# Kernel tuning notes

Hardware: AMD Instinct MI355X
Metric: run time of the kernel (lower is better)

The kernel has to match this reference:

```python
import jax, jax.numpy as jnp
import numpy as np

TEMPERATURE = 0.1
SINGLE_POS = False
EPS = 1e-8  # torch CosineSimilarity eps
B, D = 8192, 128
N_DATA = 100000


def setup_inputs() -> dict:
    key = jax.random.key(0)
    k1, k2, k3, k4 = jax.random.split(key, 4)
    features = jax.random.normal(k1, (B, D), dtype=jnp.float32)
    data_ix = jax.random.randint(k2, (B,), 0, N_DATA, dtype=jnp.int64)
    targets_t = jax.random.randint(k3, (N_DATA,), 0, 2, dtype=jnp.int64)
    targets_p = jax.random.randint(k4, (N_DATA,), 0, 2, dtype=jnp.int64)
    return {"features": features, "data_ix": data_ix,
            "targets_t": targets_t, "targets_p": targets_p}


def reference(features, data_ix, targets_t, targets_p):
    tt = targets_t[data_ix]  # [B]
    tp = targets_p[data_ix]  # [B]

    # cosine similarity matrix [B, B] (torch CosineSimilarity semantics)
    norms = jnp.linalg.norm(features, axis=1)  # [B]
    dots = features @ features.T               # [B, B]
    sim = dots / jnp.maximum(norms[:, None] * norms[None, :], EPS)
    logits = sim / TEMPERATURE                 # log(exp(sim/T)) == sim/T
    exp_sim = jnp.exp(logits)

    # pos: same true label, different predicted label; neg: reversed
    same_t = tt[:, None] == tt[None, :]
    same_p = tp[:, None] == tp[None, :]
    pos_mask = same_t & ~same_p   # excludes self automatically
    neg_mask = ~same_t & same_p

    pos_cnt = pos_mask.sum(axis=1)  # [B]
    neg_cnt = neg_mask.sum(axis=1)  # [B]

    exp_pos_sum = jnp.sum(jnp.where(pos_mask, exp_sim, 0.0), axis=1)  # [B]
    exp_neg_sum = jnp.sum(jnp.where(neg_mask, exp_sim, 0.0), axis=1)  # [B]

    if SINGLE_POS:
        # per-pair denominator: log(exp_neg_sum + exp_pos_ij)
        log_denom = jnp.log(exp_neg_sum[:, None] + exp_sim)  # [B, B]
        log_probs_sum = jnp.sum(jnp.where(pos_mask, logits - log_denom, 0.0), axis=1)
    else:
        log_denom = jnp.log(exp_neg_sum + exp_pos_sum)  # [B]
        log_probs_sum = jnp.sum(jnp.where(pos_mask, logits - log_denom[:, None], 0.0), axis=1)

    valid = (pos_cnt > 0) & (neg_cnt > 0)
    mean_log_probs = jnp.where(valid,
                               log_probs_sum / jnp.maximum(pos_cnt, 1).astype(logits.dtype),
                               0.0)
    loss = -jnp.sum(mean_log_probs) / features.shape[0]
    return loss
```

## Files before the change

### kernel.cpp

```cpp
#include <hip/hip_runtime.h>


#define NB 8192
#define ND 128
#define NIB 64
#define JS 16
#define TEMP_INV 10.0f
#define LOG2E 1.4426950408889634f
#define EXPK (TEMP_INV * LOG2E)

typedef __attribute__((ext_vector_type(8))) short short8;
typedef __attribute__((ext_vector_type(4))) float f32x4;

#define OFF_G    0
#define OFF_CLS  (NB * ND * 2)
#define OFF_CNT  (OFF_CLS + NB)
#define OFF_EPP  (OFF_CNT + 64)
#define OFF_ENP  (OFF_EPP + NB * 4 * JS)
#define OFF_LSP  (OFF_ENP + NB * 4 * JS)
#define OFF_CO   OFF_EPP
#define OFF_RL   (OFF_EPP + NB)

__device__ __forceinline__ unsigned short f2bf(float x) {
    unsigned int u = __float_as_uint(x);
    unsigned int r = (u + 0x7FFFu + ((u >> 16) & 1u)) >> 16;
    return (unsigned short)r;
}

__device__ __forceinline__ float fast_exp2(float x) {
#if __has_builtin(__builtin_amdgcn_exp2f)
    return __builtin_amdgcn_exp2f(x);
#else
    return exp2f(x);
#endif
}

typedef const __attribute__((address_space(1))) void gas_void;
typedef __attribute__((address_space(3))) void las_void;
__device__ __forceinline__ void gload_lds16(const void* g, void* s) {
    __builtin_amdgcn_global_load_lds((gas_void*)g, (las_void*)s, 16, 0, 0);
}

__global__ __launch_bounds__(256) void classify_kernel(
    const int* __restrict__ dix, const int* __restrict__ tt, const int* __restrict__ tp,
    unsigned char* __restrict__ clsO, unsigned short* __restrict__ rlocal,
    int* __restrict__ cntP, float* __restrict__ out)
{
    __shared__ int lh[4];
    const int h = blockIdx.x, tid = threadIdx.x;
    if (tid < 4) lh[tid] = 0;
    __syncthreads();
    #pragma unroll
    for (int k = 0; k < 8; ++k) {
        const int row = h * 2048 + k * 256 + tid;
        const int ix  = dix[row];
        const int c   = ((tt[ix] & 1) << 1) | (tp[ix] & 1);
        clsO[row] = (unsigned char)c;
        rlocal[row] = (unsigned short)atomicAdd(&lh[c], 1);
    }
    if (h == 0 && tid == 0) *out = 0.0f;
    __syncthreads();
    if (tid < 4) cntP[h * 4 + tid] = lh[tid];
}

__global__ __launch_bounds__(256) void normscatter_kernel(
    const float* __restrict__ F, const unsigned char* __restrict__ clsO,
    const unsigned short* __restrict__ rlocal, const int* __restrict__ cntP,
    unsigned short* __restrict__ G, unsigned char* __restrict__ clsS)
{
    const int row  = blockIdx.x * 4 + (threadIdx.x >> 6);
    const int lane = threadIdx.x & 63;
    const int c = clsO[row];
    const int h = row >> 11;
    int base = (int)rlocal[row];
    #pragma unroll
    for (int cc = 0; cc < 3; ++cc)
        if (cc < c) base += cntP[cc] + cntP[4 + cc] + cntP[8 + cc] + cntP[12 + cc];
    #pragma unroll
    for (int hh = 0; hh < 3; ++hh)
        if (hh < h) base += cntP[hh * 4 + c];

    const float2 v = *(const float2*)(F + row * ND + lane * 2);
    float ss = v.x * v.x + v.y * v.y;
    #pragma unroll
    for (int m = 1; m < 64; m <<= 1) ss += __shfl_xor(ss, m, 64);
    const float inv = rsqrtf(fmaxf(ss, 1e-24f));
    ushort2 st; st.x = f2bf(v.x * inv); st.y = f2bf(v.y * inv);
    *(ushort2*)(G + base * ND + lane * 2) = st;
    if (lane == 0) clsS[base] = (unsigned char)c;
}

__global__ __launch_bounds__(256, 4) void sim_kernel(
    const unsigned short* __restrict__ G, const unsigned char* __restrict__ clsS,
    const int* __restrict__ cntP,
    float* __restrict__ EpP, float* __restrict__ EnP, float* __restrict__ LsP)
{
    __shared__ unsigned short Blds[2][64 * 128];

    const int ib = blockIdx.x & (NIB - 1);
    const int jb = blockIdx.x >> 6;
    const int wave = threadIdx.x >> 6, lane = threadIdx.x & 63;
    const int q = lane >> 4, l16 = lane & 15;
    const int ri = ib * 128 + wave * 32;
    const int wu = __builtin_amdgcn_readfirstlane(wave);
    const int lrow4 = lane >> 4;
    const int lpos  = lane & 15;

    short8 A[2][4];
    #pragma unroll
    for (int t = 0; t < 2; ++t)
        #pragma unroll
        for (int c = 0; c < 4; ++c)
            A[t][c] = *(const short8*)(G + (ri + 16 * t + l16) * ND + c * 32 + q * 8);

    const unsigned int rcLo = *(const unsigned int*)(clsS + ri + 4 * q);
    const unsigned int rcHi = *(const unsigned int*)(clsS + ri + 16 + 4 * q);
    const int wF = clsS[ri], wL = clsS[ri + 31];
    const int bF = clsS[ib * 128], bL = clsS[ib * 128 + 127];

    float Ep[8], En[8], Ls[8];
    #pragma unroll
    for (int i = 0; i < 8; ++i) { Ep[i] = 0.f; En[i] = 0.f; Ls[i] = 0.f; }

    int cs = 0;
    #pragma unroll 1
    for (int s = 0; s < 4; ++s) {
        const int len = cntP[s] + cntP[4 + s] + cntP[8 + s] + cntP[12 + s];
        const int ce = cs + len;
        const int s1 = s ^ 1, s2 = s ^ 2;
        const bool aPb = (s1 >= bF) && (s1 <= bL);
        const bool aNb = (s2 >= bF) && (s2 <= bL);
        if (aPb || aNb) {
            const int np = (len + 63) >> 6;
            const int p0 = (jb * np) >> 4;
            const int p1 = ((jb + 1) * np) >> 4;
            if (p0 < p1) {
                float wp[8], wn[8];
                #pragma unroll
                for (int r = 0; r < 4; ++r) {
                    const int cLo = (rcLo >> (8 * r)) & 0xff;
                    const int cHi = (rcHi >> (8 * r)) & 0xff;
                    wp[r]     = (cLo == s1) ? 1.f : 0.f;
                    wp[4 + r] = (cHi == s1) ? 1.f : 0.f;
                    wn[r]     = (cLo == s2) ? 1.f : 0.f;
                    wn[4 + r] = (cHi == s2) ? 1.f : 0.f;
                }
                const bool act = ((s1 >= wF) && (s1 <= wL)) ||
                                 ((s2 >= wF) && (s2 <= wL));

                #define STAGE(BUF, P)                                              \
                    _Pragma("unroll")                                              \
                    for (int j = 0; j < 4; ++j) {                                  \
                        const int pr = wu * 16 + j * 4 + lrow4;                    \
                        int rowG = cs + (P) * 64 + pr;                             \
                        rowG = (rowG < NB - 1) ? rowG : (NB - 1);                  \
                        const int chunk = (lpos - pr) & 15;                        \
                        gload_lds16(G + rowG * ND + chunk * 8,                     \
                                    &Blds[BUF][(wu * 16 + j * 4) * ND]);           \
                    }

                STAGE(0, p0)
                __syncthreads();

                #pragma unroll 1
                for (int p = p0; p < p1; ++p) {
                    const int cur = (p - p0) & 1;
                    if (p + 1 < p1) STAGE(cur ^ 1, p + 1)
                    if (act) {
                        #pragma unroll
                        for (int st = 0; st < 4; ++st) {
                            const int j0 = cs + p * 64 + st * 16;
                            if (j0 >= ce) break;
                            short8 Bf[4];
                            #pragma unroll
                            for (int c = 0; c < 4; ++c) {
                                const int slot = (c * 4 + q + l16) & 15;
                                Bf[c] = *(const short8*)
                                    &Blds[cur][(st * 16 + l16) * ND + slot * 8];
                            }
                            f32x4 acc0 = {0.f, 0.f, 0.f, 0.f}, acc1 = {0.f, 0.f, 0.f, 0.f};
                            #pragma unroll
                            for (int c = 0; c < 4; ++c)
                                acc0 = __builtin_amdgcn_mfma_f32_16x16x32_bf16(A[0][c], Bf[c], acc0, 0, 0, 0);
                            #pragma unroll
                            for (int c = 0; c < 4; ++c)
                                acc1 = __builtin_amdgcn_mfma_f32_16x16x32_bf16(A[1][c], Bf[c], acc1, 0, 0, 0);
                            if (j0 + 16 <= ce) {
                                #pragma unroll
                                for (int r = 0; r < 4; ++r) {
                                    const float sv0 = acc0[r], sv1 = acc1[r];
                                    const float e0 = fast_exp2(sv0 * EXPK);
                                    const float e1 = fast_exp2(sv1 * EXPK);
                                    Ep[r]     = fmaf(wp[r],     e0,  Ep[r]);
                                    Ls[r]     = fmaf(wp[r],     sv0, Ls[r]);
                                    Ep[4 + r] = fmaf(wp[4 + r], e1,  Ep[4 + r]);
                                    Ls[4 + r] = fmaf(wp[4 + r], sv1, Ls[4 + r]);
                                    En[r]     = fmaf(wn[r],     e0, En[r]);
                                    En[4 + r] = fmaf(wn[4 + r], e1, En[4 + r]);
                                }
                            } else {
                                const float vm = ((j0 + l16) < ce) ? 1.f : 0.f;
                                #pragma unroll
                                for (int r = 0; r < 4; ++r) {
                                    const float sv0 = acc0[r] * vm, sv1 = acc1[r] * vm;
                                    const float e0 = fast_exp2(sv0 * EXPK) * vm;
                                    const float e1 = fast_exp2(sv1 * EXPK) * vm;
                                    Ep[r]     = fmaf(wp[r],     e0,  Ep[r]);
                                    Ls[r]     = fmaf(wp[r],     sv0, Ls[r]);
                                    Ep[4 + r] = fmaf(wp[4 + r], e1,  Ep[4 + r]);
                                    Ls[4 + r] = fmaf(wp[4 + r], sv1, Ls[4 + r]);
                                    En[r]     = fmaf(wn[r],     e0, En[r]);
                                    En[4 + r] = fmaf(wn[4 + r], e1, En[4 + r]);
                                }
                            }
                        }
                    }
                    __syncthreads();
                }
                #undef STAGE
            }
        }
        cs = ce;
    }

    #pragma unroll
    for (int m = 1; m < 16; m <<= 1)
        #pragma unroll
        for (int i = 0; i < 8; ++i) {
            Ep[i] += __shfl_xor(Ep[i], m, 64);
            En[i] += __shfl_xor(En[i], m, 64);
            Ls[i] += __shfl_xor(Ls[i], m, 64);
        }
    if (l16 == 0) {
        #pragma unroll
        for (int t = 0; t < 2; ++t)
            #pragma unroll
            for (int r = 0; r < 4; ++r) {
                const int row = ri + 16 * t + 4 * q + r;
                const int i = t * 4 + r;
                EpP[jb * NB + row] = Ep[i];
                EnP[jb * NB + row] = En[i];
                LsP[jb * NB + row] = Ls[i];
            }
    }
}

__global__ __launch_bounds__(256) void finalize_kernel(
    const float* __restrict__ EpP, const float* __restrict__ EnP,
    const float* __restrict__ LsP, const unsigned char* __restrict__ clsS,
    const int* __restrict__ cntP, float* __restrict__ out)
{
    const int i = blockIdx.x * 256 + threadIdx.x;
    const int tot0 = cntP[0] + cntP[4] + cntP[8]  + cntP[12];
    const int tot1 = cntP[1] + cntP[5] + cntP[9]  + cntP[13];
    const int tot2 = cntP[2] + cntP[6] + cntP[10] + cntP[14];
    const int tot3 = cntP[3] + cntP[7] + cntP[11] + cntP[15];
    const int c = clsS[i];
    const int pc = c ^ 1, nc = c ^ 2;
    const int pcnt = (pc == 0) ? tot0 : (pc == 1) ? tot1 : (pc == 2) ? tot2 : tot3;
    const int ncnt = (nc == 0) ? tot0 : (nc == 1) ? tot1 : (nc == 2) ? tot2 : tot3;
    float ep = 0.f, en = 0.f, ls = 0.f;
    #pragma unroll
    for (int jb = 0; jb < JS; ++jb) {
        ep += EpP[jb * NB + i];
        en += EnP[jb * NB + i];
        ls += LsP[jb * NB + i];
    }
    float contrib = 0.0f;
    if (pcnt > 0 && ncnt > 0) {
        const float ld = logf(ep + en);
        contrib = -(TEMP_INV * ls - (float)pcnt * ld) / ((float)pcnt * (float)NB);
    }
    #pragma unroll
    for (int m = 1; m < 64; m <<= 1) contrib += __shfl_xor(contrib, m, 64);
    __shared__ float wsum[4];
    if ((threadIdx.x & 63) == 0) wsum[threadIdx.x >> 6] = contrib;
    __syncthreads();
    if (threadIdx.x == 0)
        atomicAdd(out, wsum[0] + wsum[1] + wsum[2] + wsum[3]);
}

extern "C" void kernel_launch(void* const* d_in, const int* in_sizes, int n_in,
                              void* d_out, int out_size, void* d_ws, size_t ws_size,
                              hipStream_t stream) {
    const float* F = (const float*)d_in[0];
    const int* dix = (const int*)d_in[1];
    const int* tt  = (const int*)d_in[2];
    const int* tp  = (const int*)d_in[3];
    float* out = (float*)d_out;

    char* ws = (char*)d_ws;
    unsigned short* G   = (unsigned short*)(ws + OFF_G);
    unsigned char* clsS = (unsigned char*)(ws + OFF_CLS);
    int* cntP           = (int*)(ws + OFF_CNT);
    float* EpP          = (float*)(ws + OFF_EPP);
    float* EnP          = (float*)(ws + OFF_ENP);
    float* LsP          = (float*)(ws + OFF_LSP);
    unsigned char* clsO = (unsigned char*)(ws + OFF_CO);
    unsigned short* rl  = (unsigned short*)(ws + OFF_RL);

    classify_kernel<<<4, 256, 0, stream>>>(dix, tt, tp, clsO, rl, cntP, out);
    normscatter_kernel<<<2048, 256, 0, stream>>>(F, clsO, rl, cntP, G, clsS);
    sim_kernel<<<NIB * JS, 256, 0, stream>>>(G, clsS, cntP, EpP, EnP, LsP);
    finalize_kernel<<<NB / 256, 256, 0, stream>>>(EpP, EnP, LsP, clsS, cntP, out);
}
```

Baseline: 124.4 us.

## Specialize sim kernel per wave class, single-buffer LDS, widen classify grid

The class-accumulation inner loop becomes a templated routine. Waves whose 32 rows share one class use a specialized mode that accumulates only the needed sums, with no mask FMAs. LDS staging drops from double buffering to a single buffer with a sync per panel, and occupancy hints change to waves_per_eu(3,4), trading load/compute overlap for lower LDS use and more resident blocks. The classify kernel now runs 8 blocks of 1024 threads, one row per thread, and the count-prefix logic is updated to match.

```diff
diff --git a/kernel.cpp b/kernel.cpp
--- a/kernel.cpp
+++ b/kernel.cpp
@@ -5,6 +5,7 @@
 #define ND 128
 #define NIB 64
 #define JS 16
+#define NH 8
 #define TEMP_INV 10.0f
 #define LOG2E 1.4426950408889634f
 #define EXPK (TEMP_INV * LOG2E)
@@ -15,7 +16,7 @@
 #define OFF_G    0
 #define OFF_CLS  (NB * ND * 2)
 #define OFF_CNT  (OFF_CLS + NB)
-#define OFF_EPP  (OFF_CNT + 64)
+#define OFF_EPP  (OFF_CNT + 128)
 #define OFF_ENP  (OFF_EPP + NB * 4 * JS)
 #define OFF_LSP  (OFF_ENP + NB * 4 * JS)
 #define OFF_CO   OFF_EPP
@@ -41,7 +42,7 @@
     __builtin_amdgcn_global_load_lds((gas_void*)g, (las_void*)s, 16, 0, 0);
 }
 
-__global__ __launch_bounds__(256) void classify_kernel(
+__global__ __launch_bounds__(1024) void classify_kernel(
     const int* __restrict__ dix, const int* __restrict__ tt, const int* __restrict__ tp,
     unsigned char* __restrict__ clsO, unsigned short* __restrict__ rlocal,
     int* __restrict__ cntP, float* __restrict__ out)
@@ -50,14 +51,11 @@
     const int h = blockIdx.x, tid = threadIdx.x;
     if (tid < 4) lh[tid] = 0;
     __syncthreads();
-    #pragma unroll
-    for (int k = 0; k < 8; ++k) {
-        const int row = h * 2048 + k * 256 + tid;
-        const int ix  = dix[row];
-        const int c   = ((tt[ix] & 1) << 1) | (tp[ix] & 1);
-        clsO[row] = (unsigned char)c;
-        rlocal[row] = (unsigned short)atomicAdd(&lh[c], 1);
-    }
+    const int row = h * 1024 + tid;
+    const int ix  = dix[row];
+    const int c   = ((tt[ix] & 1) << 1) | (tp[ix] & 1);
+    clsO[row] = (unsigned char)c;
+    rlocal[row] = (unsigned short)atomicAdd(&lh[c], 1);
     if (h == 0 && tid == 0) *out = 0.0f;
     __syncthreads();
     if (tid < 4) cntP[h * 4 + tid] = lh[tid];
@@ -71,13 +69,16 @@
     const int row  = blockIdx.x * 4 + (threadIdx.x >> 6);
     const int lane = threadIdx.x & 63;
     const int c = clsO[row];
-    const int h = row >> 11;
+    const int h = row >> 10;
     int base = (int)rlocal[row];
     #pragma unroll
     for (int cc = 0; cc < 3; ++cc)
-        if (cc < c) base += cntP[cc] + cntP[4 + cc] + cntP[8 + cc] + cntP[12 + cc];
-    #pragma unroll
-    for (int hh = 0; hh < 3; ++hh)
+        if (cc < c) {
+            #pragma unroll
+            for (int hh = 0; hh < NH; ++hh) base += cntP[hh * 4 + cc];
+        }
+    #pragma unroll
+    for (int hh = 0; hh < NH - 1; ++hh)
         if (hh < h) base += cntP[hh * 4 + c];
 
     const float2 v = *(const float2*)(F + row * ND + lane * 2);
@@ -90,12 +91,107 @@
     if (lane == 0) clsS[base] = (unsigned char)c;
 }
 
-__global__ __launch_bounds__(256, 4) void sim_kernel(
+__device__ __forceinline__ void stage_panel(
+    const unsigned short* __restrict__ G, unsigned short* Blds,
+    int rbase, int wu, int lrow4, int lpos)
+{
+    #pragma unroll
+    for (int j = 0; j < 4; ++j) {
+        const int pr = wu * 16 + j * 4 + lrow4;
+        int rowG = rbase + pr;
+        rowG = (rowG < NB - 1) ? rowG : (NB - 1);
+        const int chunk = (lpos - pr) & 15;
+        gload_lds16(G + rowG * ND + chunk * 8, Blds + (wu * 16 + j * 4) * ND);
+    }
+}
+
+template<int MODE>
+__device__ __forceinline__ void seg_panels(
+    const unsigned short* __restrict__ G, unsigned short* Blds,
+    const short8 (&A)[2][4],
+    float (&Ep)[8], float (&En)[8], float (&Ls)[8],
+    const float (&wp)[8], const float (&wn)[8],
+    int cs, int ce, int p0, int p1, int wu, int lane)
+{
+    const int lrow4 = lane >> 4, lpos = lane & 15;
+    const int q = lane >> 4, l16 = lane & 15;
+    #pragma unroll 1
+    for (int p = p0; p < p1; ++p) {
+        stage_panel(G, Blds, cs + p * 64, wu, lrow4, lpos);
+        __syncthreads();
+        if (MODE != 0) {
+            #pragma unroll
+            for (int st = 0; st < 4; ++st) {
+                const int j0 = cs + p * 64 + st * 16;
+                if (j0 >= ce) break;
+                short8 Bf[4];
+                #pragma unroll
+                for (int c = 0; c < 4; ++c) {
+                    const int slot = (c * 4 + q + l16) & 15;
+                    Bf[c] = *(const short8*)&Blds[(st * 16 + l16) * ND + slot * 8];
+                }
+                f32x4 acc0 = {0.f, 0.f, 0.f, 0.f}, acc1 = {0.f, 0.f, 0.f, 0.f};
+                #pragma unroll
+                for (int c = 0; c < 4; ++c)
+                    acc0 = __builtin_amdgcn_mfma_f32_16x16x32_bf16(A[0][c], Bf[c], acc0, 0, 0, 0);
+                #pragma unroll
+                for (int c = 0; c < 4; ++c)
+                    acc1 = __builtin_amdgcn_mfma_f32_16x16x32_bf16(A[1][c], Bf[c], acc1, 0, 0, 0);
+                if (j0 + 16 <= ce) {
+                    #pragma unroll
+                    for (int r = 0; r < 4; ++r) {
+                        const float sv0 = acc0[r], sv1 = acc1[r];
+                        const float e0 = fast_exp2(sv0 * EXPK);
+                        const float e1 = fast_exp2(sv1 * EXPK);
+                        if (MODE == 1) {
+                            Ep[r] += e0;      Ls[r] += sv0;
+                            Ep[4 + r] += e1;  Ls[4 + r] += sv1;
+                        } else if (MODE == 2) {
+                            En[r] += e0;      En[4 + r] += e1;
+                        } else {
+                            Ep[r]     = fmaf(wp[r],     e0,  Ep[r]);
+                            Ls[r]     = fmaf(wp[r],     sv0, Ls[r]);
+                            Ep[4 + r] = fmaf(wp[4 + r], e1,  Ep[4 + r]);
+                            Ls[4 + r] = fmaf(wp[4 + r], sv1, Ls[4 + r]);
+                            En[r]     = fmaf(wn[r],     e0, En[r]);
+                            En[4 + r] = fmaf(wn[4 + r], e1, En[4 + r]);
+                        }
+                    }
+                } else {
+                    const float vm = ((j0 + l16) < ce) ? 1.f : 0.f;
+                    #pragma unroll
+                    for (int r = 0; r < 4; ++r) {
+                        const float sv0 = acc0[r] * vm, sv1 = acc1[r] * vm;
+                        const float e0 = fast_exp2(sv0 * EXPK) * vm;
+                        const float e1 = fast_exp2(sv1 * EXPK) * vm;
+                        if (MODE == 1) {
+                            Ep[r] += e0;      Ls[r] += sv0;
+                            Ep[4 + r] += e1;  Ls[4 + r] += sv1;
+                        } else if (MODE == 2) {
+                            En[r] += e0;      En[4 + r] += e1;
+                        } else {
+                            Ep[r]     = fmaf(wp[r],     e0,  Ep[r]);
+                            Ls[r]     = fmaf(wp[r],     sv0, Ls[r]);
+                            Ep[4 + r] = fmaf(wp[4 + r], e1,  Ep[4 + r]);
+                            Ls[4 + r] = fmaf(wp[4 + r], sv1, Ls[4 + r]);
+                            En[r]     = fmaf(wn[r],     e0, En[r]);
+                            En[4 + r] = fmaf(wn[4 + r], e1, En[4 + r]);
+                        }
+                    }
+                }
+            }
+        }
+        __syncthreads();
+    }
+}
+
+__global__ __launch_bounds__(256) __attribute__((amdgpu_waves_per_eu(3, 4)))
+void sim_kernel(
     const unsigned short* __restrict__ G, const unsigned char* __restrict__ clsS,
     const int* __restrict__ cntP,
     float* __restrict__ EpP, float* __restrict__ EnP, float* __restrict__ LsP)
 {
-    __shared__ unsigned short Blds[2][64 * 128];
+    __shared__ unsigned short Blds[64 * 128];
 
     const int ib = blockIdx.x & (NIB - 1);
     const int jb = blockIdx.x >> 6;
@@ -103,8 +199,6 @@
     const int q = lane >> 4, l16 = lane & 15;
     const int ri = ib * 128 + wave * 32;
     const int wu = __builtin_amdgcn_readfirstlane(wave);
-    const int lrow4 = lane >> 4;
-    const int lpos  = lane & 15;
 
     short8 A[2][4];
     #pragma unroll
@@ -121,11 +215,14 @@
     float Ep[8], En[8], Ls[8];
     #pragma unroll
     for (int i = 0; i < 8; ++i) { Ep[i] = 0.f; En[i] = 0.f; Ls[i] = 0.f; }
+    float wp[8], wn[8];
 
     int cs = 0;
     #pragma unroll 1
     for (int s = 0; s < 4; ++s) {
-        const int len = cntP[s] + cntP[4 + s] + cntP[8 + s] + cntP[12 + s];
+        int len = 0;
+        #pragma unroll
+        for (int h = 0; h < NH; ++h) len += cntP[h * 4 + s];
         const int ce = cs + len;
         const int s1 = s ^ 1, s2 = s ^ 2;
         const bool aPb = (s1 >= bF) && (s1 <= bL);
@@ -135,89 +232,25 @@
             const int p0 = (jb * np) >> 4;
             const int p1 = ((jb + 1) * np) >> 4;
             if (p0 < p1) {
-                float wp[8], wn[8];
-                #pragma unroll
-                for (int r = 0; r < 4; ++r) {
-                    const int cLo = (rcLo >> (8 * r)) & 0xff;
-                    const int cHi = (rcHi >> (8 * r)) & 0xff;
-                    wp[r]     = (cLo == s1) ? 1.f : 0.f;
-                    wp[4 + r] = (cHi == s1) ? 1.f : 0.f;
-                    wn[r]     = (cLo == s2) ? 1.f : 0.f;
-                    wn[4 + r] = (cHi == s2) ? 1.f : 0.f;
+                if (wF == wL) {
+                    if (s1 == wF)
+                        seg_panels<1>(G, Blds, A, Ep, En, Ls, wp, wn, cs, ce, p0, p1, wu, lane);
+                    else if (s2 == wF)
+                        seg_panels<2>(G, Blds, A, Ep, En, Ls, wp, wn, cs, ce, p0, p1, wu, lane);
+                    else
+                        seg_panels<0>(G, Blds, A, Ep, En, Ls, wp, wn, cs, ce, p0, p1, wu, lane);
+                } else {
+                    #pragma unroll
+                    for (int r = 0; r < 4; ++r) {
+                        const int cLo = (rcLo >> (8 * r)) & 0xff;
+                        const int cHi = (rcHi >> (8 * r)) & 0xff;
+                        wp[r]     = (cLo == s1) ? 1.f : 0.f;
+                        wp[4 + r] = (cHi == s1) ? 1.f : 0.f;
+                        wn[r]     = (cLo == s2) ? 1.f : 0.f;
+                        wn[4 + r] = (cHi == s2) ? 1.f : 0.f;
+                    }
+                    seg_panels<3>(G, Blds, A, Ep, En, Ls, wp, wn, cs, ce, p0, p1, wu, lane);
                 }
-                const bool act = ((s1 >= wF) && (s1 <= wL)) ||
-                                 ((s2 >= wF) && (s2 <= wL));
-
-                #define STAGE(BUF, P)                                              \
-                    _Pragma("unroll")                                              \
-                    for (int j = 0; j < 4; ++j) {                                  \
-                        const int pr = wu * 16 + j * 4 + lrow4;                    \
-                        int rowG = cs + (P) * 64 + pr;                             \
-                        rowG = (rowG < NB - 1) ? rowG : (NB - 1);                  \
-                        const int chunk = (lpos - pr) & 15;                        \
-                        gload_lds16(G + rowG * ND + chunk * 8,                     \
-                                    &Blds[BUF][(wu * 16 + j * 4) * ND]);           \
-                    }
-
-                STAGE(0, p0)
-                __syncthreads();
-
-                #pragma unroll 1
-                for (int p = p0; p < p1; ++p) {
-                    const int cur = (p - p0) & 1;
-                    if (p + 1 < p1) STAGE(cur ^ 1, p + 1)
-                    if (act) {
-                        #pragma unroll
-                        for (int st = 0; st < 4; ++st) {
-                            const int j0 = cs + p * 64 + st * 16;
-                            if (j0 >= ce) break;
-                            short8 Bf[4];
-                            #pragma unroll
-                            for (int c = 0; c < 4; ++c) {
-                                const int slot = (c * 4 + q + l16) & 15;
-                                Bf[c] = *(const short8*)
-                                    &Blds[cur][(st * 16 + l16) * ND + slot * 8];
-                            }
-                            f32x4 acc0 = {0.f, 0.f, 0.f, 0.f}, acc1 = {0.f, 0.f, 0.f, 0.f};
-                            #pragma unroll
-                            for (int c = 0; c < 4; ++c)
-                                acc0 = __builtin_amdgcn_mfma_f32_16x16x32_bf16(A[0][c], Bf[c], acc0, 0, 0, 0);
-                            #pragma unroll
-                            for (int c = 0; c < 4; ++c)
-                                acc1 = __builtin_amdgcn_mfma_f32_16x16x32_bf16(A[1][c], Bf[c], acc1, 0, 0, 0);
-                            if (j0 + 16 <= ce) {
-                                #pragma unroll
-                                for (int r = 0; r < 4; ++r) {
-                                    const float sv0 = acc0[r], sv1 = acc1[r];
-                                    const float e0 = fast_exp2(sv0 * EXPK);
-                                    const float e1 = fast_exp2(sv1 * EXPK);
-                                    Ep[r]     = fmaf(wp[r],     e0,  Ep[r]);
-                                    Ls[r]     = fmaf(wp[r],     sv0, Ls[r]);
-                                    Ep[4 + r] = fmaf(wp[4 + r], e1,  Ep[4 + r]);
-                                    Ls[4 + r] = fmaf(wp[4 + r], sv1, Ls[4 + r]);
-                                    En[r]     = fmaf(wn[r],     e0, En[r]);
-                                    En[4 + r] = fmaf(wn[4 + r], e1, En[4 + r]);
-                                }
-                            } else {
-                                const float vm = ((j0 + l16) < ce) ? 1.f : 0.f;
-                                #pragma unroll
-                                for (int r = 0; r < 4; ++r) {
-                                    const float sv0 = acc0[r] * vm, sv1 = acc1[r] * vm;
-                                    const float e0 = fast_exp2(sv0 * EXPK) * vm;
-                                    const float e1 = fast_exp2(sv1 * EXPK) * vm;
-                                    Ep[r]     = fmaf(wp[r],     e0,  Ep[r]);
-                                    Ls[r]     = fmaf(wp[r],     sv0, Ls[r]);
-                                    Ep[4 + r] = fmaf(wp[4 + r], e1,  Ep[4 + r]);
-                                    Ls[4 + r] = fmaf(wp[4 + r], sv1, Ls[4 + r]);
-                                    En[r]     = fmaf(wn[r],     e0, En[r]);
-                                    En[4 + r] = fmaf(wn[4 + r], e1, En[4 + r]);
-                                }
-                            }
-                        }
-                    }
-                    __syncthreads();
-                }
-                #undef STAGE
             }
         }
         cs = ce;
@@ -251,14 +284,15 @@
     const int* __restrict__ cntP, float* __restrict__ out)
 {
     const int i = blockIdx.x * 256 + threadIdx.x;
-    const int tot0 = cntP[0] + cntP[4] + cntP[8]  + cntP[12];
-    const int tot1 = cntP[1] + cntP[5] + cntP[9]  + cntP[13];
-    const int tot2 = cntP[2] + cntP[6] + cntP[10] + cntP[14];
-    const int tot3 = cntP[3] + cntP[7] + cntP[11] + cntP[15];
+    int tot[4] = {0, 0, 0, 0};
+    #pragma unroll
+    for (int hh = 0; hh < NH; ++hh)
+        #pragma unroll
+        for (int cc = 0; cc < 4; ++cc) tot[cc] += cntP[hh * 4 + cc];
     const int c = clsS[i];
     const int pc = c ^ 1, nc = c ^ 2;
-    const int pcnt = (pc == 0) ? tot0 : (pc == 1) ? tot1 : (pc == 2) ? tot2 : tot3;
-    const int ncnt = (nc == 0) ? tot0 : (nc == 1) ? tot1 : (nc == 2) ? tot2 : tot3;
+    const int pcnt = (pc == 0) ? tot[0] : (pc == 1) ? tot[1] : (pc == 2) ? tot[2] : tot[3];
+    const int ncnt = (nc == 0) ? tot[0] : (nc == 1) ? tot[1] : (nc == 2) ? tot[2] : tot[3];
     float ep = 0.f, en = 0.f, ls = 0.f;
     #pragma unroll
     for (int jb = 0; jb < JS; ++jb) {
@@ -299,7 +333,7 @@
     unsigned char* clsO = (unsigned char*)(ws + OFF_CO);
     unsigned short* rl  = (unsigned short*)(ws + OFF_RL);
 
-    classify_kernel<<<4, 256, 0, stream>>>(dix, tt, tp, clsO, rl, cntP, out);
+    classify_kernel<<<NH, 1024, 0, stream>>>(dix, tt, tp, clsO, rl, cntP, out);
     normscatter_kernel<<<2048, 256, 0, stream>>>(F, clsO, rl, cntP, G, clsS);
     sim_kernel<<<NIB * JS, 256, 0, stream>>>(G, clsS, cntP, EpP, EnP, LsP);
     finalize_kernel<<<NB / 256, 256, 0, stream>>>(EpP, EnP, LsP, clsS, cntP, out);
```

After: 103.2 us. 17.1% less time.
